# Optimization experiments

Hardware: AMD Instinct MI355X
Metric: run time of the kernel (lower is better)

Reference implementation:

```python
import math
import jax, jax.numpy as jnp
import numpy as np

# hyperparameters (module defaults; w_scale overridden to 1.0)
EMA_SPEED = 0.05
REW_SENS = 1.0
LR = 0.0033
MOMENTUM = 0.4
UNTANH = 0.6
SPEED = 0.5
WIDTH = 0.1
WD = 0.01
LAT_DECAY = 0.01
NOISE_SCALE = 0.8
C_MOMENT = 0.99
W_SCALE = 1.0


def rms_norm(x, axis=-1):
    return x * jax.lax.rsqrt(jnp.mean(x * x, axis=axis, keepdims=True) + 1e-6)


def setup_inputs() -> dict:
    key = jax.random.key(0)
    ks = jax.random.split(key, 16)
    B, N, D = 16, 128, 64
    s = 1.0 / math.sqrt(D)
    return {
        'eye_env': jax.random.normal(ks[0], (B, D), jnp.float32),
        'stomach_env': jax.random.normal(ks[1], (B, D), jnp.float32),
        'state': jax.random.normal(ks[2], (B, N, D), jnp.float32),
        'output': jax.random.normal(ks[3], (B, N, D), jnp.float32),
        'W1': jax.random.normal(ks[4], (B, N, D, D), jnp.float32) * s,
        'W2': jax.random.normal(ks[5], (B, N, D, D), jnp.float32) * s,
        'W3': jax.random.normal(ks[6], (B, N, D, D), jnp.float32) * s,
        'M1': jax.random.normal(ks[7], (B, N, D, D), jnp.float32) * 0.2,
        'M2': jax.random.normal(ks[8], (B, N, D, D), jnp.float32) * 0.2,
        'M3': jax.random.normal(ks[9], (B, N, D, D), jnp.float32) * 0.2,
        'E_baseline': jax.random.uniform(ks[10], (B, N, D), jnp.float32),
        'A': jax.nn.softmax(jax.random.normal(ks[11], (B, N, N), jnp.float32), axis=2),
        'noise_A': jax.random.normal(ks[12], (B, N, N), jnp.float32),
        'noise1_raw': jax.random.normal(ks[13], (B, N, D), jnp.float32),
        'noise2_raw': jax.random.normal(ks[14], (B, N, D), jnp.float32),
        'step_counter': 0,
    }


def reference(eye_env, stomach_env, state, output, W1, W2, W3, M1, M2, M3,
              E_baseline, A, noise_A, noise1_raw, noise2_raw, step_counter):
    B, N, D = state.shape
    sc = jnp.float32(step_counter) + 1.0  # self.step_counter += 1

    # attention routing
    q = jnp.einsum('bnj,bnjk->bnk', state, W3)
    k = jnp.einsum('bnj,bnjk->bnk', state, W2)
    raw_A = jnp.einsum('bnd,bmd->bnm', q, k) / math.sqrt(D) + noise_A * 1e-5
    P_dense = jax.nn.softmax(raw_A, axis=2)
    keep = (P_dense > 1.0 / (N + 1.0)) | (P_dense == jnp.max(P_dense, axis=2, keepdims=True))
    P = jax.nn.softmax(jnp.where(keep, raw_A, -jnp.inf), axis=2)
    A_new = A * C_MOMENT + P * (1.0 - C_MOMENT)
    A_new = A_new.at[:, 0:2, :].set(0.0)

    # message passing + sensory clamp
    target = jnp.einsum('bnm,bmd->bnd', A_new, output)
    target = target.at[:, 0].set(eye_env).at[:, 1].set(stomach_env)

    # prediction
    raw_pred = jnp.einsum('bnj,bnjk->bnk', state, W1)
    raw = raw_pred - jnp.tanh(raw_pred) * UNTANH
    prediction = jnp.tanh(raw) * math.sqrt(2.0 + math.sqrt(2.0))

    err = prediction - target
    E_curr = jax.nn.softmax(err, axis=-1)
    bmask = (E_baseline == 0).astype(jnp.float32)
    Eb = E_baseline * (1.0 - bmask) + E_curr * bmask
    Eb = Eb * (1.0 - EMA_SPEED) + EMA_SPEED * E_curr
    advantage = E_curr - Eb
    R = -rms_norm(advantage[..., None] * REW_SENS)  # (B,N,D,1)
    mask = (Eb > 0).astype(jnp.float32)[..., None]

    # noise injection
    state_mag = jnp.sum(jnp.abs(state), axis=(-2, -1), keepdims=True)
    noise1 = noise1_raw / (1.0 + state_mag)
    noise2 = noise2_raw * jnp.std(err, ddof=1) * NOISE_SCALE
    noisy_state = state + noise1 + noise2

    # Hebbian outer-product gradient, G_NORM=1.0 -> rms-normalized
    lg = -jnp.einsum('bni,bnj->bnij', err, noisy_state)
    lg = rms_norm(lg, axis=(2, 3))

    plasticity = 1.0 - R
    grad1 = plasticity * lg * mask + LAT_DECAY * W3 - WD * W1
    grad2 = plasticity * lg * mask + LAT_DECAY * W1 - WD * W2
    grad3 = plasticity * lg * mask + LAT_DECAY * W2 - WD * W3

    # travelling gaussian column mask
    idx = jnp.arange(D, dtype=jnp.float32).reshape(1, 1, 1, D)
    center = (sc * SPEED) % D
    diff = jnp.abs(idx - center)
    diff = jnp.minimum(diff, D - diff)
    g_mask = jnp.exp(-diff ** 2 / (2.0 * WIDTH ** 2 + 1e-6))

    M1n = M1 * MOMENTUM + (1.0 - MOMENTUM) * (grad1 * g_mask)
    M2n = M2 * MOMENTUM + (1.0 - MOMENTUM) * (grad2 * g_mask)
    M3n = M3 * MOMENTUM + (1.0 - MOMENTUM) * (grad3 * g_mask)
    W1n = rms_norm(W1 + LR * M1n) * W_SCALE
    W2n = rms_norm(W2 + LR * M2n) * W_SCALE
    W3n = rms_norm(W3 + LR * M3n) * W_SCALE

    # new output = prediction, new state = target
    return prediction, target, A_new, W1n, W2n, W3n
```

## Files before the change

kernel.cpp:

```cpp
#include <hip/hip_runtime.h>
#include <hip/hip_bf16.h>

typedef __hip_bfloat16 bf16;
typedef float f32x4 __attribute__((ext_vector_type(4)));

__device__ __forceinline__ float b2f(bf16 x) { return __bfloat162float(x); }

template<bool F32>
__device__ __forceinline__ float ld(const void* p, size_t i) {
  if constexpr (F32) return ((const float*)p)[i];
  else return b2f(((const bf16*)p)[i]);
}

template<bool F32>
__device__ __forceinline__ void ld4(const void* p, size_t i, float v[4]) {
  if constexpr (F32) {
    const float4 a = *(const float4*)((const float*)p + i);
    v[0]=a.x; v[1]=a.y; v[2]=a.z; v[3]=a.w;
  } else {
    union { uint2 u; bf16 h[4]; } t;
    t.u = *(const uint2*)((const bf16*)p + i);
    #pragma unroll
    for (int c = 0; c < 4; ++c) v[c] = b2f(t.h[c]);
  }
}

template<bool F32>
__device__ __forceinline__ void ld8(const void* p, size_t i, float v[8]) {
  if constexpr (F32) {
    const float4 a = *(const float4*)((const float*)p + i);
    const float4 b = *(const float4*)((const float*)p + i + 4);
    v[0]=a.x; v[1]=a.y; v[2]=a.z; v[3]=a.w;
    v[4]=b.x; v[5]=b.y; v[6]=b.z; v[7]=b.w;
  } else {
    union { uint4 u; bf16 h[8]; } t;
    t.u = *(const uint4*)((const bf16*)p + i);
    #pragma unroll
    for (int c = 0; c < 8; ++c) v[c] = b2f(t.h[c]);
  }
}

template<bool F32>
__device__ __forceinline__ void ld8nt(const void* p, size_t i, float v[8]) {
  if constexpr (F32) {
    const f32x4* q = (const f32x4*)((const float*)p + i);
    const f32x4 a = __builtin_nontemporal_load(q);
    const f32x4 b = __builtin_nontemporal_load(q + 1);
    v[0]=a[0]; v[1]=a[1]; v[2]=a[2]; v[3]=a[3];
    v[4]=b[0]; v[5]=b[1]; v[6]=b[2]; v[7]=b[3];
  } else {
    ld8<false>(p, i, v);
  }
}

__device__ __forceinline__ float plast(float Ec, float Ebl) {
  const float Eb0 = (Ebl == 0.f) ? Ec : Ebl;
  const float Eb  = Eb0 * 0.95f + 0.05f * Ec;
  const float adv = Ec - Eb;
  const float R   = -adv * rsqrtf(adv*adv + 1e-6f);
  return (Eb > 0.f) ? (1.f - R) : 0.f;
}


template<bool F32>
__device__ __forceinline__ void k1_body(
    const void* state, const void* W1, const void* W2, const void* W3,
    float* qw, float* kw, float* mag, float* out_pred,
    float* s_state, float* s_part)
{
  const int node = blockIdx.x;
  const int b = node >> 7;
  const int tid = threadIdx.x;
  const int w = tid >> 6, lane = tid & 63;
  const int jg = lane >> 4, cq = lane & 15;
  const int c0 = cq * 4;
  const size_t nb = (size_t)node * 4096;

  float w3v[4][4], w2v[4][4], w1v[4][4];
  #pragma unroll
  for (int jj = 0; jj < 4; ++jj) {
    const int j = w*16 + jg*4 + jj;
    const size_t o = nb + (size_t)j*64 + c0;
    ld4<F32>(W3, o, w3v[jj]);
    ld4<F32>(W2, o, w2v[jj]);
    ld4<F32>(W1, o, w1v[jj]);
  }
  if (tid < 64) s_state[tid] = ld<F32>(state, (size_t)node*64 + tid);
  __syncthreads();

  float aq[4] = {0,0,0,0}, ak[4] = {0,0,0,0}, ap[4] = {0,0,0,0};
  #pragma unroll
  for (int jj = 0; jj < 4; ++jj) {
    const float sj = s_state[w*16 + jg*4 + jj];
    #pragma unroll
    for (int cc = 0; cc < 4; ++cc) {
      aq[cc] += sj * w3v[jj][cc];
      ak[cc] += sj * w2v[jj][cc];
      ap[cc] += sj * w1v[jj][cc];
    }
  }
  #pragma unroll
  for (int cc = 0; cc < 4; ++cc) {
    aq[cc] += __shfl_xor(aq[cc], 16, 64); aq[cc] += __shfl_xor(aq[cc], 32, 64);
    ak[cc] += __shfl_xor(ak[cc], 16, 64); ak[cc] += __shfl_xor(ak[cc], 32, 64);
    ap[cc] += __shfl_xor(ap[cc], 16, 64); ap[cc] += __shfl_xor(ap[cc], 32, 64);
  }
  if (jg == 0) {
    *(float4*)&s_part[w*192 +  0 + c0] = make_float4(aq[0], aq[1], aq[2], aq[3]);
    *(float4*)&s_part[w*192 + 64 + c0] = make_float4(ak[0], ak[1], ak[2], ak[3]);
    *(float4*)&s_part[w*192 +128 + c0] = make_float4(ap[0], ap[1], ap[2], ap[3]);
  }
  if (w == 3) {
    float a = fabsf(s_state[lane]);
    #pragma unroll
    for (int s = 32; s; s >>= 1) a += __shfl_xor(a, s, 64);
    if (lane == 0) atomicAdd(&mag[b], a);
  }
  __syncthreads();
  if (tid < 192) {
    const int mat = tid >> 6, col = tid & 63;
    const float v = s_part[0*192 + mat*64 + col] + s_part[1*192 + mat*64 + col]
                  + s_part[2*192 + mat*64 + col] + s_part[3*192 + mat*64 + col];
    if (mat == 0)      qw[(size_t)node*64 + col] = v;
    else if (mat == 1) kw[(size_t)node*64 + col] = v;
    else {
      const float raw  = v - tanhf(v) * 0.6f;
      out_pred[(size_t)node*64 + col] = tanhf(raw) * 1.8477590650225735f;
    }
  }
}

__global__ __launch_bounds__(256) void k1_qkpred(
    const void* __restrict__ state,
    const void* __restrict__ W1, const void* __restrict__ W2,
    const void* __restrict__ W3,
    float* __restrict__ qw, float* __restrict__ kw,
    float* __restrict__ mag, float* __restrict__ out_pred,
    int* __restrict__ flagws)
{
  __shared__ alignas(16) float s_state[64];
  __shared__ alignas(16) float s_part[768];
  __shared__ int s_flag;
  const int tid = threadIdx.x;
  bool huge = false;
  for (int i = tid; i < 1024; i += 256) {
    const float x = b2f(((const bf16*)state)[i]);
    if (!(fabsf(x) < 1e5f)) huge = true;
  }
  const unsigned long long m = __ballot(huge);
  if (tid == 0) s_flag = 0;
  __syncthreads();
  if ((tid & 63) == 0 && m != 0ull) s_flag = 1;
  __syncthreads();
  const bool f32 = (s_flag != 0);
  if (blockIdx.x == 0 && tid == 0) *flagws = f32 ? 1 : 0;
  if (f32) k1_body<true >(state, W1, W2, W3, qw, kw, mag, out_pred, s_state, s_part);
  else     k1_body<false>(state, W1, W2, W3, qw, kw, mag, out_pred, s_state, s_part);
}

template<bool F32>
__device__ __forceinline__ void k2_body(
    const float* qw, const float* kw, const float* predw,
    const void* noiseA, const void* Aold, const void* outp,
    const void* eye, const void* stomach, const void* Ebase,
    float* errw, float* plw, float* stats,
    float* out_target, float* out_A,
    float* s_k, float* s_q, float* s_A)
{
  const int bidx = blockIdx.x;
  const int b = bidx >> 4;
  const int n0 = (bidx & 15) * 8;
  const int tid = threadIdx.x;

  {
    const float* kwb = kw + (size_t)b * 8192;
    #pragma unroll
    for (int it = 0; it < 8; ++it) {
      const int idx = it*256 + tid;
      const int m = idx >> 4, dq = idx & 15;
      const float4 v = *(const float4*)(kwb + (size_t)idx * 4);
      float* dst = &s_k[m*65 + dq*4];
      dst[0] = v.x; dst[1] = v.y; dst[2] = v.z; dst[3] = v.w;
    }
    if (tid < 128) {
      const int rr = tid >> 4, dq = tid & 15;
      *(float4*)&s_q[rr*64 + dq*4] =
          *(const float4*)(qw + ((size_t)(b*128 + n0 + rr))*64 + dq*4);
    }
  }
  __syncthreads();

  const int rr = tid >> 5, c = tid & 31;
  const int n = n0 + rr;
  const size_t node = (size_t)b*128 + n;

  float acc[4] = {0.f, 0.f, 0.f, 0.f};
  {
    const float* qrow = s_q + rr*64;
    #pragma unroll 8
    for (int j = 0; j < 64; ++j) {
      const float qv = qrow[j];
      acc[0] += qv * s_k[(c     )*65 + j];
      acc[1] += qv * s_k[(c + 32)*65 + j];
      acc[2] += qv * s_k[(c + 64)*65 + j];
      acc[3] += qv * s_k[(c + 96)*65 + j];
    }
  }
  float raw[4];
  #pragma unroll
  for (int i = 0; i < 4; ++i)
    raw[i] = acc[i]*0.125f + 1e-5f*ld<F32>(noiseA, node*128 + c + 32*i);

  float rmx = fmaxf(fmaxf(raw[0], raw[1]), fmaxf(raw[2], raw[3]));
  #pragma unroll
  for (int s = 16; s >= 1; s >>= 1) rmx = fmaxf(rmx, __shfl_xor(rmx, s, 64));
  float e[4], S = 0.f;
  #pragma unroll
  for (int i = 0; i < 4; ++i) { e[i] = expf(raw[i] - rmx); S += e[i]; }
  #pragma unroll
  for (int s = 16; s >= 1; s >>= 1) S += __shfl_xor(S, s, 64);
  float ek[4], Sk = 0.f;
  #pragma unroll
  for (int i = 0; i < 4; ++i) {
    const float Pd = e[i] / S;
    ek[i] = ((Pd > 0.007751937984496124f) || (raw[i] == rmx)) ? e[i] : 0.f;
    Sk += ek[i];
  }
  #pragma unroll
  for (int s = 16; s >= 1; s >>= 1) Sk += __shfl_xor(Sk, s, 64);
  #pragma unroll
  for (int i = 0; i < 4; ++i) {
    const int m = c + 32*i;
    const float P = ek[i] / Sk;
    const float An = (n < 2) ? 0.f
                   : 0.99f * ld<F32>(Aold, node*128 + m) + 0.01f * P;
    out_A[node*128 + m] = An;
    s_A[rr*128 + m] = An;
  }
  __syncthreads();

  float t0, t1;
  if (n == 0) {
    t0 = ld<F32>(eye, (size_t)b*64 + c);
    t1 = ld<F32>(eye, (size_t)b*64 + c + 32);
  } else if (n == 1) {
    t0 = ld<F32>(stomach, (size_t)b*64 + c);
    t1 = ld<F32>(stomach, (size_t)b*64 + c + 32);
  } else {
    t0 = 0.f; t1 = 0.f;
    const float* arow = s_A + rr*128;
    const size_t ob = (size_t)b * 8192;
    #pragma unroll 4
    for (int m = 0; m < 128; ++m) {
      const float a = arow[m];
      t0 += a * ld<F32>(outp, ob + m*64 + c);
      t1 += a * ld<F32>(outp, ob + m*64 + c + 32);
    }
  }
  out_target[node*64 + c]      = t0;
  out_target[node*64 + c + 32] = t1;
  const float e0 = predw[node*64 + c]      - t0;
  const float e1 = predw[node*64 + c + 32] - t1;
  errw[node*64 + c]      = e0;
  errw[node*64 + c + 32] = e1;

  float mx = fmaxf(e0, e1);
  #pragma unroll
  for (int s = 16; s >= 1; s >>= 1) mx = fmaxf(mx, __shfl_xor(mx, s, 64));
  const float x0 = expf(e0 - mx), x1 = expf(e1 - mx);
  float ss = x0 + x1;
  #pragma unroll
  for (int s = 16; s >= 1; s >>= 1) ss += __shfl_xor(ss, s, 64);
  plw[node*64 + c]      = plast(x0/ss, ld<F32>(Ebase, node*64 + c));
  plw[node*64 + c + 32] = plast(x1/ss, ld<F32>(Ebase, node*64 + c + 32));

  float se = e0 + e1, sq = e0*e0 + e1*e1;
  #pragma unroll
  for (int s = 16; s >= 1; s >>= 1) { se += __shfl_xor(se, s, 64); sq += __shfl_xor(sq, s, 64); }
  if (c == 0) { atomicAdd(&stats[0], se); atomicAdd(&stats[1], sq); }
}

__global__ __launch_bounds__(256) void k2_attn(
    const int* __restrict__ flag,
    const float* __restrict__ qw, const float* __restrict__ kw,
    const float* __restrict__ predw,
    const void* __restrict__ noiseA, const void* __restrict__ Aold,
    const void* __restrict__ outp,
    const void* __restrict__ eye, const void* __restrict__ stomach,
    const void* __restrict__ Ebase,
    float* __restrict__ errw, float* __restrict__ plw,
    float* __restrict__ stats,
    float* __restrict__ out_target, float* __restrict__ out_A)
{
  __shared__ alignas(16) float s_k[128*65];
  __shared__ alignas(16) float s_q[8*64];
  __shared__ alignas(16) float s_A[8*128];
  if (*flag) k2_body<true >(qw,kw,predw,noiseA,Aold,outp,eye,stomach,Ebase,errw,plw,stats,out_target,out_A,s_k,s_q,s_A);
  else       k2_body<false>(qw,kw,predw,noiseA,Aold,outp,eye,stomach,Ebase,errw,plw,stats,out_target,out_A,s_k,s_q,s_A);
}

template<bool F32>
__device__ __forceinline__ void k3_body(
    const float* errw, const float* plw,
    const void* state, const void* n1raw, const void* n2raw,
    const float* mag, const float* stats, const int* stepc,
    const void* W1, const void* W2, const void* W3,
    const void* M1, const void* M2, const void* M3,
    float* oW1, float* oW2, float* oW3,
    float* s_err, float* s_ns, float* s_pe, float* s_c, float* s_g)
{
  const int node = blockIdx.x;
  const int b = node >> 7;
  const int tid = threadIdx.x;
  if (tid < 64) {
    const float e = errw[(size_t)node*64 + tid];
    s_err[tid] = e;
    s_pe[tid]  = plw[(size_t)node*64 + tid] * e;
  } else if (tid < 128) {
    const int i = tid - 64;
    const float S1 = stats[0], S2 = stats[1];
    const float Mn = 131072.f;
    const float var = (S2 - S1*S1/Mn) / (Mn - 1.f);
    const float stdv = sqrtf(fmaxf(var, 0.f));
    s_ns[i] = ld<F32>(state, (size_t)node*64 + i)
            + ld<F32>(n1raw, (size_t)node*64 + i) / (1.f + mag[b])
            + ld<F32>(n2raw, (size_t)node*64 + i) * stdv * 0.8f;
  } else if (tid < 192) {
    const int i = tid - 128;
    const float sc = (float)stepc[0] + 1.f;
    const float center = fmodf(sc * 0.5f, 64.f);
    float diff = fabsf((float)i - center);
    diff = fminf(diff, 64.f - diff);
    s_g[i] = expf(-diff*diff * (1.f/0.020001f));
  }

  const int r = tid >> 3;
  const int l8 = tid & 7;
  const size_t off = (size_t)node*4096 + (size_t)r*64 + (size_t)l8*8;
  float w1v[8], w2v[8], w3v[8], m1v[8], m2v[8], m3v[8];
  ld8  <F32>(W1, off, w1v); ld8  <F32>(W2, off, w2v); ld8  <F32>(W3, off, w3v);
  ld8nt<F32>(M1, off, m1v); ld8nt<F32>(M2, off, m2v); ld8nt<F32>(M3, off, m3v);
  __syncthreads();

  if (tid < 64) {
    float e2 = s_err[tid]*s_err[tid];
    float n2 = s_ns[tid]*s_ns[tid];
    #pragma unroll
    for (int s = 32; s; s >>= 1) { e2 += __shfl_xor(e2, s, 64); n2 += __shfl_xor(n2, s, 64); }
    s_c[tid] = -s_ns[tid] * rsqrtf(e2 * n2 * (1.f/4096.f) + 1e-6f);
  }
  __syncthreads();

  const float pe = s_pe[r];
  float t1[8], t2[8], t3[8];
  float ss1 = 0.f, ss2 = 0.f, ss3 = 0.f;
  #pragma unroll
  for (int cc = 0; cc < 8; ++cc) {
    const int j = l8*8 + cc;
    const float lgterm = pe * s_c[j];
    const float g = s_g[j];
    const float g1 = lgterm + 0.01f*w3v[cc] - 0.01f*w1v[cc];
    const float g2 = lgterm + 0.01f*w1v[cc] - 0.01f*w2v[cc];
    const float g3 = lgterm + 0.01f*w2v[cc] - 0.01f*w3v[cc];
    const float v1 = w1v[cc] + 0.0033f*(0.4f*m1v[cc] + 0.6f*g1*g);
    const float v2 = w2v[cc] + 0.0033f*(0.4f*m2v[cc] + 0.6f*g2*g);
    const float v3 = w3v[cc] + 0.0033f*(0.4f*m3v[cc] + 0.6f*g3*g);
    t1[cc] = v1; t2[cc] = v2; t3[cc] = v3;
    ss1 += v1*v1; ss2 += v2*v2; ss3 += v3*v3;
  }
  #pragma unroll
  for (int s = 1; s <= 4; s <<= 1) {
    ss1 += __shfl_xor(ss1, s, 64);
    ss2 += __shfl_xor(ss2, s, 64);
    ss3 += __shfl_xor(ss3, s, 64);
  }
  const float r1 = rsqrtf(ss1*(1.f/64.f) + 1e-6f);
  const float r2 = rsqrtf(ss2*(1.f/64.f) + 1e-6f);
  const float r3 = rsqrtf(ss3*(1.f/64.f) + 1e-6f);
  f32x4 o;
  o[0]=t1[0]*r1; o[1]=t1[1]*r1; o[2]=t1[2]*r1; o[3]=t1[3]*r1;
  __builtin_nontemporal_store(o, (f32x4*)(oW1 + off));
  o[0]=t1[4]*r1; o[1]=t1[5]*r1; o[2]=t1[6]*r1; o[3]=t1[7]*r1;
  __builtin_nontemporal_store(o, (f32x4*)(oW1 + off + 4));
  o[0]=t2[0]*r2; o[1]=t2[1]*r2; o[2]=t2[2]*r2; o[3]=t2[3]*r2;
  __builtin_nontemporal_store(o, (f32x4*)(oW2 + off));
  o[0]=t2[4]*r2; o[1]=t2[5]*r2; o[2]=t2[6]*r2; o[3]=t2[7]*r2;
  __builtin_nontemporal_store(o, (f32x4*)(oW2 + off + 4));
  o[0]=t3[0]*r3; o[1]=t3[1]*r3; o[2]=t3[2]*r3; o[3]=t3[3]*r3;
  __builtin_nontemporal_store(o, (f32x4*)(oW3 + off));
  o[0]=t3[4]*r3; o[1]=t3[5]*r3; o[2]=t3[6]*r3; o[3]=t3[7]*r3;
  __builtin_nontemporal_store(o, (f32x4*)(oW3 + off + 4));
}

__global__ __launch_bounds__(512, 2) void k3_update(
    const int* __restrict__ flag,
    const float* __restrict__ errw, const float* __restrict__ plw,
    const void* __restrict__ state, const void* __restrict__ n1raw,
    const void* __restrict__ n2raw,
    const float* __restrict__ mag, const float* __restrict__ stats,
    const int* __restrict__ stepc,
    const void* __restrict__ W1, const void* __restrict__ W2,
    const void* __restrict__ W3,
    const void* __restrict__ M1, const void* __restrict__ M2,
    const void* __restrict__ M3,
    float* __restrict__ oW1, float* __restrict__ oW2, float* __restrict__ oW3)
{
  __shared__ alignas(16) float s_err[64], s_ns[64], s_pe[64], s_c[64], s_g[64];
  if (*flag) k3_body<true >(errw,plw,state,n1raw,n2raw,mag,stats,stepc,W1,W2,W3,M1,M2,M3,oW1,oW2,oW3,s_err,s_ns,s_pe,s_c,s_g);
  else       k3_body<false>(errw,plw,state,n1raw,n2raw,mag,stats,stepc,W1,W2,W3,M1,M2,M3,oW1,oW2,oW3,s_err,s_ns,s_pe,s_c,s_g);
}

extern "C" void kernel_launch(void* const* d_in, const int* in_sizes, int n_in,
                              void* d_out, int out_size, void* d_ws, size_t ws_size,
                              hipStream_t stream) {
  const void* eye     = d_in[0];
  const void* stomach = d_in[1];
  const void* state   = d_in[2];
  const void* outp    = d_in[3];
  const void* W1      = d_in[4];
  const void* W2      = d_in[5];
  const void* W3      = d_in[6];
  const void* M1      = d_in[7];
  const void* M2      = d_in[8];
  const void* M3      = d_in[9];
  const void* Ebase   = d_in[10];
  const void* Aold    = d_in[11];
  const void* noiseA  = d_in[12];
  const void* n1raw   = d_in[13];
  const void* n2raw   = d_in[14];
  const int*  stepc   = (const int*)d_in[15];

  float* ws    = (float*)d_ws;
  float* qw    = ws;
  float* kw    = ws + 131072;
  float* errw  = ws + 262144;
  float* plw   = ws + 393216;
  float* mag   = ws + 524288;
  float* stats = ws + 524304;
  int*   flag  = (int*)(ws + 524306);

  float* out        = (float*)d_out;
  float* out_pred   = out;
  float* out_target = out + 131072;
  float* out_A      = out + 262144;
  float* oW1        = out + 524288;
  float* oW2        = out + 8912896;
  float* oW3        = out + 17301504;

  hipMemsetAsync(mag, 0, 18 * sizeof(float), stream);
  k1_qkpred<<<2048, 256, 0, stream>>>(state, W1, W2, W3, qw, kw, mag, out_pred, flag);
  k2_attn<<<256, 256, 0, stream>>>(flag, qw, kw, out_pred, noiseA, Aold, outp,
                                   eye, stomach, Ebase, errw, plw, stats,
                                   out_target, out_A);
  k3_update<<<2048, 512, 0, stream>>>(flag, errw, plw, state, n1raw, n2raw, mag, stats,
                                      stepc, W1, W2, W3, M1, M2, M3, oW1, oW2, oW3);
}
```

Before: 348.3 us.

## Use wave-per-node k1 and shuffle-based k3 prologue, drop shared memory barriers

```diff
diff --git a/kernel.cpp b/kernel.cpp
--- a/kernel.cpp
+++ b/kernel.cpp
@@ -63,41 +63,36 @@
 
 
 template<bool F32>
-__device__ __forceinline__ void k1_body(
+__device__ __forceinline__ void k1_wave(
     const void* state, const void* W1, const void* W2, const void* W3,
-    float* qw, float* kw, float* mag, float* out_pred,
-    float* s_state, float* s_part)
-{
-  const int node = blockIdx.x;
+    float* qw, float* kw, float* mag, float* out_pred, int node, int lane)
+{
   const int b = node >> 7;
-  const int tid = threadIdx.x;
-  const int w = tid >> 6, lane = tid & 63;
+  const float st = ld<F32>(state, (size_t)node*64 + lane);
+  float am = fabsf(st);
+  #pragma unroll
+  for (int s = 32; s; s >>= 1) am += __shfl_xor(am, s, 64);
+  if (lane == 0) atomicAdd(&mag[b], am);
+
   const int jg = lane >> 4, cq = lane & 15;
   const int c0 = cq * 4;
   const size_t nb = (size_t)node * 4096;
-
-  float w3v[4][4], w2v[4][4], w1v[4][4];
-  #pragma unroll
-  for (int jj = 0; jj < 4; ++jj) {
-    const int j = w*16 + jg*4 + jj;
+  float aq[4] = {0,0,0,0}, ak[4] = {0,0,0,0}, ap[4] = {0,0,0,0};
+  #pragma unroll 4
+  for (int jj = 0; jj < 16; ++jj) {
+    const int j = jg*16 + jj;
+    const float sj = __shfl(st, j, 64);
     const size_t o = nb + (size_t)j*64 + c0;
-    ld4<F32>(W3, o, w3v[jj]);
-    ld4<F32>(W2, o, w2v[jj]);
-    ld4<F32>(W1, o, w1v[jj]);
-  }
-  if (tid < 64) s_state[tid] = ld<F32>(state, (size_t)node*64 + tid);
-  __syncthreads();
-
-  float aq[4] = {0,0,0,0}, ak[4] = {0,0,0,0}, ap[4] = {0,0,0,0};
-  #pragma unroll
-  for (int jj = 0; jj < 4; ++jj) {
-    const float sj = s_state[w*16 + jg*4 + jj];
-    #pragma unroll
-    for (int cc = 0; cc < 4; ++cc) {
-      aq[cc] += sj * w3v[jj][cc];
-      ak[cc] += sj * w2v[jj][cc];
-      ap[cc] += sj * w1v[jj][cc];
-    }
+    float wv[4];
+    ld4<F32>(W3, o, wv);
+    #pragma unroll
+    for (int cc = 0; cc < 4; ++cc) aq[cc] += sj * wv[cc];
+    ld4<F32>(W2, o, wv);
+    #pragma unroll
+    for (int cc = 0; cc < 4; ++cc) ak[cc] += sj * wv[cc];
+    ld4<F32>(W1, o, wv);
+    #pragma unroll
+    for (int cc = 0; cc < 4; ++cc) ap[cc] += sj * wv[cc];
   }
   #pragma unroll
   for (int cc = 0; cc < 4; ++cc) {
@@ -106,27 +101,17 @@
     ap[cc] += __shfl_xor(ap[cc], 16, 64); ap[cc] += __shfl_xor(ap[cc], 32, 64);
   }
   if (jg == 0) {
-    *(float4*)&s_part[w*192 +  0 + c0] = make_float4(aq[0], aq[1], aq[2], aq[3]);
-    *(float4*)&s_part[w*192 + 64 + c0] = make_float4(ak[0], ak[1], ak[2], ak[3]);
-    *(float4*)&s_part[w*192 +128 + c0] = make_float4(ap[0], ap[1], ap[2], ap[3]);
-  }
-  if (w == 3) {
-    float a = fabsf(s_state[lane]);
-    #pragma unroll
-    for (int s = 32; s; s >>= 1) a += __shfl_xor(a, s, 64);
-    if (lane == 0) atomicAdd(&mag[b], a);
-  }
-  __syncthreads();
-  if (tid < 192) {
-    const int mat = tid >> 6, col = tid & 63;
-    const float v = s_part[0*192 + mat*64 + col] + s_part[1*192 + mat*64 + col]
-                  + s_part[2*192 + mat*64 + col] + s_part[3*192 + mat*64 + col];
-    if (mat == 0)      qw[(size_t)node*64 + col] = v;
-    else if (mat == 1) kw[(size_t)node*64 + col] = v;
-    else {
-      const float raw  = v - tanhf(v) * 0.6f;
-      out_pred[(size_t)node*64 + col] = tanhf(raw) * 1.8477590650225735f;
+    *(float4*)(qw + (size_t)node*64 + c0) = make_float4(aq[0], aq[1], aq[2], aq[3]);
+  } else if (jg == 1) {
+    *(float4*)(kw + (size_t)node*64 + c0) = make_float4(ak[0], ak[1], ak[2], ak[3]);
+  } else if (jg == 2) {
+    float pr[4];
+    #pragma unroll
+    for (int cc = 0; cc < 4; ++cc) {
+      const float raw = ap[cc] - tanhf(ap[cc]) * 0.6f;
+      pr[cc] = tanhf(raw) * 1.8477590650225735f;
     }
+    *(float4*)(out_pred + (size_t)node*64 + c0) = make_float4(pr[0], pr[1], pr[2], pr[3]);
   }
 }
 
@@ -138,24 +123,18 @@
     float* __restrict__ mag, float* __restrict__ out_pred,
     int* __restrict__ flagws)
 {
-  __shared__ alignas(16) float s_state[64];
-  __shared__ alignas(16) float s_part[768];
-  __shared__ int s_flag;
   const int tid = threadIdx.x;
+  const int w = tid >> 6, lane = tid & 63;
   bool huge = false;
-  for (int i = tid; i < 1024; i += 256) {
+  for (int i = lane; i < 1024; i += 64) {
     const float x = b2f(((const bf16*)state)[i]);
     if (!(fabsf(x) < 1e5f)) huge = true;
   }
-  const unsigned long long m = __ballot(huge);
-  if (tid == 0) s_flag = 0;
-  __syncthreads();
-  if ((tid & 63) == 0 && m != 0ull) s_flag = 1;
-  __syncthreads();
-  const bool f32 = (s_flag != 0);
+  const bool f32 = (__ballot(huge) != 0ull);
   if (blockIdx.x == 0 && tid == 0) *flagws = f32 ? 1 : 0;
-  if (f32) k1_body<true >(state, W1, W2, W3, qw, kw, mag, out_pred, s_state, s_part);
-  else     k1_body<false>(state, W1, W2, W3, qw, kw, mag, out_pred, s_state, s_part);
+  const int node = blockIdx.x * 4 + w;
+  if (f32) k1_wave<true >(state, W1, W2, W3, qw, kw, mag, out_pred, node, lane);
+  else     k1_wave<false>(state, W1, W2, W3, qw, kw, mag, out_pred, node, lane);
 }
 
 template<bool F32>
@@ -306,59 +285,60 @@
     const float* mag, const float* stats, const int* stepc,
     const void* W1, const void* W2, const void* W3,
     const void* M1, const void* M2, const void* M3,
-    float* oW1, float* oW2, float* oW3,
-    float* s_err, float* s_ns, float* s_pe, float* s_c, float* s_g)
+    float* oW1, float* oW2, float* oW3)
 {
   const int node = blockIdx.x;
   const int b = node >> 7;
   const int tid = threadIdx.x;
-  if (tid < 64) {
-    const float e = errw[(size_t)node*64 + tid];
-    s_err[tid] = e;
-    s_pe[tid]  = plw[(size_t)node*64 + tid] * e;
-  } else if (tid < 128) {
-    const int i = tid - 64;
-    const float S1 = stats[0], S2 = stats[1];
-    const float Mn = 131072.f;
-    const float var = (S2 - S1*S1/Mn) / (Mn - 1.f);
-    const float stdv = sqrtf(fmaxf(var, 0.f));
-    s_ns[i] = ld<F32>(state, (size_t)node*64 + i)
-            + ld<F32>(n1raw, (size_t)node*64 + i) / (1.f + mag[b])
-            + ld<F32>(n2raw, (size_t)node*64 + i) * stdv * 0.8f;
-  } else if (tid < 192) {
-    const int i = tid - 128;
-    const float sc = (float)stepc[0] + 1.f;
-    const float center = fmodf(sc * 0.5f, 64.f);
-    float diff = fabsf((float)i - center);
-    diff = fminf(diff, 64.f - diff);
-    s_g[i] = expf(-diff*diff * (1.f/0.020001f));
-  }
-
+  const int lane = tid & 63;
   const int r = tid >> 3;
   const int l8 = tid & 7;
+
+  const size_t sb = (size_t)node*64 + lane;
+  const float e_i  = errw[sb];
+  const float pl_i = plw[sb];
+  const float st_i = ld<F32>(state, sb);
+  const float n1_i = ld<F32>(n1raw, sb);
+  const float n2_i = ld<F32>(n2raw, sb);
+  const float magb = mag[b];
+  const float S1 = stats[0], S2 = stats[1];
+  const float scv = (float)stepc[0] + 1.f;
+
   const size_t off = (size_t)node*4096 + (size_t)r*64 + (size_t)l8*8;
   float w1v[8], w2v[8], w3v[8], m1v[8], m2v[8], m3v[8];
   ld8  <F32>(W1, off, w1v); ld8  <F32>(W2, off, w2v); ld8  <F32>(W3, off, w3v);
   ld8nt<F32>(M1, off, m1v); ld8nt<F32>(M2, off, m2v); ld8nt<F32>(M3, off, m3v);
-  __syncthreads();
-
-  if (tid < 64) {
-    float e2 = s_err[tid]*s_err[tid];
-    float n2 = s_ns[tid]*s_ns[tid];
-    #pragma unroll
-    for (int s = 32; s; s >>= 1) { e2 += __shfl_xor(e2, s, 64); n2 += __shfl_xor(n2, s, 64); }
-    s_c[tid] = -s_ns[tid] * rsqrtf(e2 * n2 * (1.f/4096.f) + 1e-6f);
-  }
-  __syncthreads();
-
-  const float pe = s_pe[r];
+
+  const float Mn = 131072.f;
+  const float var = (S2 - S1*S1/Mn) / (Mn - 1.f);
+  const float stdv = sqrtf(fmaxf(var, 0.f));
+  const float ns_i = st_i + n1_i / (1.f + magb)
+                   + n2_i * stdv * 0.8f;
+  float e2 = e_i*e_i, q2 = ns_i*ns_i;
+  #pragma unroll
+  for (int s = 32; s; s >>= 1) { e2 += __shfl_xor(e2, s, 64); q2 += __shfl_xor(q2, s, 64); }
+  const float c_i  = -ns_i * rsqrtf(e2 * q2 * (1.f/4096.f) + 1e-6f);
+  const float pe_i = pl_i * e_i;
+  const float center = fmodf(scv * 0.5f, 64.f);
+  float dff = fabsf((float)lane - center);
+  dff = fminf(dff, 64.f - dff);
+  const float g_i = expf(-dff*dff * (1.f/0.020001f));
+
+  const float pe = __shfl(pe_i, r, 64);
+  float cj[8], gj[8];
+  #pragma unroll
+  for (int cc = 0; cc < 8; ++cc) {
+    const int j = l8*8 + cc;
+    cj[cc] = __shfl(c_i, j, 64);
+    gj[cc] = __shfl(g_i, j, 64);
+  }
+
   float t1[8], t2[8], t3[8];
   float ss1 = 0.f, ss2 = 0.f, ss3 = 0.f;
   #pragma unroll
   for (int cc = 0; cc < 8; ++cc) {
-    const int j = l8*8 + cc;
-    const float lgterm = pe * s_c[j];
-    const float g = s_g[j];
+    const float lgterm = pe * cj[cc];
+    const float g = gj[cc];
     const float g1 = lgterm + 0.01f*w3v[cc] - 0.01f*w1v[cc];
     const float g2 = lgterm + 0.01f*w1v[cc] - 0.01f*w2v[cc];
     const float g3 = lgterm + 0.01f*w2v[cc] - 0.01f*w3v[cc];
@@ -377,22 +357,15 @@
   const float r1 = rsqrtf(ss1*(1.f/64.f) + 1e-6f);
   const float r2 = rsqrtf(ss2*(1.f/64.f) + 1e-6f);
   const float r3 = rsqrtf(ss3*(1.f/64.f) + 1e-6f);
-  f32x4 o;
-  o[0]=t1[0]*r1; o[1]=t1[1]*r1; o[2]=t1[2]*r1; o[3]=t1[3]*r1;
-  __builtin_nontemporal_store(o, (f32x4*)(oW1 + off));
-  o[0]=t1[4]*r1; o[1]=t1[5]*r1; o[2]=t1[6]*r1; o[3]=t1[7]*r1;
-  __builtin_nontemporal_store(o, (f32x4*)(oW1 + off + 4));
-  o[0]=t2[0]*r2; o[1]=t2[1]*r2; o[2]=t2[2]*r2; o[3]=t2[3]*r2;
-  __builtin_nontemporal_store(o, (f32x4*)(oW2 + off));
-  o[0]=t2[4]*r2; o[1]=t2[5]*r2; o[2]=t2[6]*r2; o[3]=t2[7]*r2;
-  __builtin_nontemporal_store(o, (f32x4*)(oW2 + off + 4));
-  o[0]=t3[0]*r3; o[1]=t3[1]*r3; o[2]=t3[2]*r3; o[3]=t3[3]*r3;
-  __builtin_nontemporal_store(o, (f32x4*)(oW3 + off));
-  o[0]=t3[4]*r3; o[1]=t3[5]*r3; o[2]=t3[6]*r3; o[3]=t3[7]*r3;
-  __builtin_nontemporal_store(o, (f32x4*)(oW3 + off + 4));
-}
-
-__global__ __launch_bounds__(512, 2) void k3_update(
+  *(float4*)(oW1 + off)     = make_float4(t1[0]*r1, t1[1]*r1, t1[2]*r1, t1[3]*r1);
+  *(float4*)(oW1 + off + 4) = make_float4(t1[4]*r1, t1[5]*r1, t1[6]*r1, t1[7]*r1);
+  *(float4*)(oW2 + off)     = make_float4(t2[0]*r2, t2[1]*r2, t2[2]*r2, t2[3]*r2);
+  *(float4*)(oW2 + off + 4) = make_float4(t2[4]*r2, t2[5]*r2, t2[6]*r2, t2[7]*r2);
+  *(float4*)(oW3 + off)     = make_float4(t3[0]*r3, t3[1]*r3, t3[2]*r3, t3[3]*r3);
+  *(float4*)(oW3 + off + 4) = make_float4(t3[4]*r3, t3[5]*r3, t3[6]*r3, t3[7]*r3);
+}
+
+__global__ __launch_bounds__(512) void k3_update(
     const int* __restrict__ flag,
     const float* __restrict__ errw, const float* __restrict__ plw,
     const void* __restrict__ state, const void* __restrict__ n1raw,
@@ -405,9 +378,8 @@
     const void* __restrict__ M3,
     float* __restrict__ oW1, float* __restrict__ oW2, float* __restrict__ oW3)
 {
-  __shared__ alignas(16) float s_err[64], s_ns[64], s_pe[64], s_c[64], s_g[64];
-  if (*flag) k3_body<true >(errw,plw,state,n1raw,n2raw,mag,stats,stepc,W1,W2,W3,M1,M2,M3,oW1,oW2,oW3,s_err,s_ns,s_pe,s_c,s_g);
-  else       k3_body<false>(errw,plw,state,n1raw,n2raw,mag,stats,stepc,W1,W2,W3,M1,M2,M3,oW1,oW2,oW3,s_err,s_ns,s_pe,s_c,s_g);
+  if (*flag) k3_body<true >(errw,plw,state,n1raw,n2raw,mag,stats,stepc,W1,W2,W3,M1,M2,M3,oW1,oW2,oW3);
+  else       k3_body<false>(errw,plw,state,n1raw,n2raw,mag,stats,stepc,W1,W2,W3,M1,M2,M3,oW1,oW2,oW3);
 }
 
 extern "C" void kernel_launch(void* const* d_in, const int* in_sizes, int n_in,
@@ -448,7 +420,7 @@
   float* oW3        = out + 17301504;
 
   hipMemsetAsync(mag, 0, 18 * sizeof(float), stream);
-  k1_qkpred<<<2048, 256, 0, stream>>>(state, W1, W2, W3, qw, kw, mag, out_pred, flag);
+  k1_qkpred<<<512, 256, 0, stream>>>(state, W1, W2, W3, qw, kw, mag, out_pred, flag);
   k2_attn<<<256, 256, 0, stream>>>(flag, qw, kw, out_pred, noiseA, Aold, outp,
                                    eye, stomach, Ebase, errw, plw, stats,
                                    out_target, out_A);
```

Measured after the change: 358.6 us. 1.03x slower.
